# Kernel optimization log

Measured on AMD Instinct MI355X. Metric: run time of the kernel, lower is better.

## Reference

```python
import jax, jax.numpy as jnp
import numpy as np

B, S, D, H, HD, FF, L = 16384, 5, 6, 2, 3, 2048, 4
EPS = 1e-5


def setup_inputs() -> dict:
    key = jax.random.key(0)
    ks = jax.random.split(key, 20)
    s = lambda fan: 1.0 / np.sqrt(fan)
    inp = {
        'x': jax.random.normal(ks[0], (B, S, D), dtype=jnp.float32),
        # per-layer stacked MHA params (in_proj split into q/k/v) and out_proj
        'Wq': jax.random.uniform(ks[1], (L, D, D), jnp.float32, -s(D), s(D)),
        'bq': jax.random.uniform(ks[2], (L, D), jnp.float32, -s(D), s(D)),
        'Wk': jax.random.uniform(ks[3], (L, D, D), jnp.float32, -s(D), s(D)),
        'bk': jax.random.uniform(ks[4], (L, D), jnp.float32, -s(D), s(D)),
        'Wv': jax.random.uniform(ks[5], (L, D, D), jnp.float32, -s(D), s(D)),
        'bv': jax.random.uniform(ks[6], (L, D), jnp.float32, -s(D), s(D)),
        'Wo': jax.random.uniform(ks[7], (L, D, D), jnp.float32, -s(D), s(D)),
        'bo': jax.random.uniform(ks[8], (L, D), jnp.float32, -s(D), s(D)),
        # FFN: linear1 D->FF, linear2 FF->D (torch Linear stores [out,in])
        'W1': jax.random.uniform(ks[9], (L, FF, D), jnp.float32, -s(D), s(D)),
        'b1': jax.random.uniform(ks[10], (L, FF), jnp.float32, -s(D), s(D)),
        'W2': jax.random.uniform(ks[11], (L, D, FF), jnp.float32, -s(FF), s(FF)),
        'b2': jax.random.uniform(ks[12], (L, D), jnp.float32, -s(FF), s(FF)),
        # layernorms
        'g1': jnp.ones((L, D), jnp.float32),
        'be1': jnp.zeros((L, D), jnp.float32),
        'g2': jnp.ones((L, D), jnp.float32),
        'be2': jnp.zeros((L, D), jnp.float32),
        # classification head Linear(30, 2)
        'Wfc': jax.random.uniform(ks[13], (2, S * D), jnp.float32, -s(S * D), s(S * D)),
        'bfc': jax.random.uniform(ks[14], (2,), jnp.float32, -s(S * D), s(S * D)),
    }
    return inp


def _layernorm(x, g, b):
    m = jnp.mean(x, axis=-1, keepdims=True)
    v = jnp.mean(jnp.square(x - m), axis=-1, keepdims=True)
    return (x - m) * jax.lax.rsqrt(v + EPS) * g + b


def _encoder_stack(x, Wq, bq, Wk, bk, Wv, bv, Wo, bo, W1, b1, W2, b2, g1, be1, g2, be2):
    scale = 1.0 / np.sqrt(HD)
    for i in range(L):  # small fixed loop over layers
        # multi-head self-attention (post-norm, eval mode: dropout = identity)
        q = (x @ Wq[i].T + bq[i]).reshape(B, S, H, HD)
        k = (x @ Wk[i].T + bk[i]).reshape(B, S, H, HD)
        v = (x @ Wv[i].T + bv[i]).reshape(B, S, H, HD)
        scores = jnp.einsum('bqhd,bkhd->bhqk', q, k) * scale
        attn = jax.nn.softmax(scores, axis=-1)
        ctx = jnp.einsum('bhqk,bkhd->bqhd', attn, v).reshape(B, S, D)
        x = _layernorm(x + ctx @ Wo[i].T + bo[i], g1[i], be1[i])
        # FFN: relu(x W1^T + b1) W2^T + b2
        h = jax.nn.relu(x @ W1[i].T + b1[i])  # [B,S,FF]
        x = _layernorm(x + h @ W2[i].T + b2[i], g2[i], be2[i])
    return x


def reference(x, Wq, bq, Wk, bk, Wv, bv, Wo, bo, W1, b1, W2, b2, g1, be1, g2, be2, Wfc, bfc):
    t = _encoder_stack(x, Wq, bq, Wk, bk, Wv, bv, Wo, bo, W1, b1, W2, b2, g1, be1, g2, be2)
    flat = t.reshape(-1, S * D)
    logits = flat @ Wfc.T + bfc
    return jax.nn.softmax(logits, axis=1)
```

## Files before the change

### kernel.cpp

```cpp
#include <hip/hip_runtime.h>
#include <math.h>

#define NL 4
#define NBATCH 16384
#define NS 5
#define ND 6
#define NH 2
#define NHD 3
#define NFF 2048
#define EPSV 1e-5f

#define ITEMS 32
#define TPB 512
#define NPAIR 64
#define ROW (NS * ND)
#define NVAL (ITEMS * ROW)
#define HROWS 80

typedef __fp16 v8h __attribute__((ext_vector_type(8)));
typedef __fp16 v2h __attribute__((ext_vector_type(2)));
typedef float f32x4 __attribute__((ext_vector_type(4)));

union HU8 { uint4 u; v8h h; __fp16 f[8]; };

__device__ inline unsigned pk_u32(float a, float b) {
    union { v2h h; unsigned u; } x;
    x.h = __builtin_amdgcn_cvt_pkrtz(a, b);
    return x.u;
}

__device__ __align__(16) uint4 W1A[NL * NPAIR * 64];
__device__ __align__(16) uint4 W1B[NL * NPAIR * 64];
__device__ __align__(16) uint4 W2P[NL * NPAIR * 64];

__global__ void pack_kernel(const float* __restrict__ W1,
                            const float* __restrict__ b1,
                            const float* __restrict__ W2) {
    const int TOT = NL * NPAIR * 64;
    int idx = blockIdx.x * 256 + threadIdx.x;
    if (idx >= 3 * TOT) return;
    int arr = idx / TOT, t = idx - arr * TOT;
    int lane = t & 63, p = (t >> 6) & 63, l = t >> 12;
    int r = lane & 15, g = lane >> 4;
    HU8 o; o.u = make_uint4(0u, 0u, 0u, 0u);
    if (arr < 2) {
        if (g == 0) {
            int j = (2 * p + arr) * 16 + r;
#pragma unroll
            for (int e = 0; e < ND; ++e)
                o.f[e] = (__fp16)W1[(size_t)(l * NFF + j) * ND + e];
            o.f[6] = (__fp16)b1[l * NFF + j];
            o.f[7] = (__fp16)0.f;
        }
        if (arr == 0) W1A[t] = o.u; else W1B[t] = o.u;
    } else {
        if (r < ND) {
#pragma unroll
            for (int e = 0; e < 8; ++e) {
                int j = p * 32 + ((e < 4) ? (4 * g + e) : (16 + 4 * g + e - 4));
                o.f[e] = (__fp16)W2[(size_t)(l * ND + r) * NFF + j];
            }
        }
        W2P[t] = o.u;
    }
}

__global__ __launch_bounds__(TPB, 4) void encoder_kernel(
    const float* __restrict__ xin,
    const float* __restrict__ Wq, const float* __restrict__ bq,
    const float* __restrict__ Wk, const float* __restrict__ bk,
    const float* __restrict__ Wv, const float* __restrict__ bv,
    const float* __restrict__ Wo, const float* __restrict__ bo,
    const float* __restrict__ b2,
    const float* __restrict__ g1, const float* __restrict__ be1,
    const float* __restrict__ g2, const float* __restrict__ be2,
    const float* __restrict__ Wfc, const float* __restrict__ bfc,
    float* __restrict__ out) {
    __shared__ float xs[NVAL];
    __shared__ float ybuf[2 * 4 * 5 * 32 * 4];
    __shared__ float kvs[2 * 16 * NS * 12];

    const int tid = threadIdx.x;
    const int base = blockIdx.x * ITEMS;

    if (tid < NVAL / 4)
        ((float4*)xs)[tid] = ((const float4*)(xin + (size_t)base * ROW))[tid];

    const int lane = tid & 63;
    const int w = tid >> 6;
    const int jq = w & 3;
    const int c16 = lane & 15, g = lane >> 4;
    const int tid2 = tid & 255;
    const int aiL = tid2 >> 4;
    const int u = tid2 & 15;

    v8h z8; z8 = (v8h)(__fp16)0.f;
    const f32x4 cz = {0.f, 0.f, 0.f, 0.f};

    for (int k = 0; k <= 9; ++k) {
        __syncthreads();
        if (w < 4) {
            if (k >= 1 && k <= 8) {
                const int hf = (k - 1) & 1, lf = (k - 1) >> 1;
                const uint4* pw1a = W1A + (size_t)(lf * NPAIR + jq * 16) * 64 + lane;
                const uint4* pw1b = W1B + (size_t)(lf * NPAIR + jq * 16) * 64 + lane;
                const uint4* pw2  = W2P + (size_t)(lf * NPAIR + jq * 16) * 64 + lane;
                uint4 wpf[2][6];
#pragma unroll
                for (int pp = 0; pp < 2; ++pp) {
                    wpf[0][pp * 3 + 0] = pw1a[pp * 64];
                    wpf[0][pp * 3 + 1] = pw1b[pp * 64];
                    wpf[0][pp * 3 + 2] = pw2[pp * 64];
                }
                v8h xb[5];
#pragma unroll
                for (int mt = 0; mt < 5; ++mt) {
                    HU8 ux; ux.u = make_uint4(0u, 0u, 0u, 0u);
                    if (g == 0) {
                        int row = hf * HROWS + mt * 16 + c16;
                        const float* xp = &xs[row * ND];
                        ux.u.x = pk_u32(xp[0], xp[1]);
                        ux.u.y = pk_u32(xp[2], xp[3]);
                        ux.u.z = pk_u32(xp[4], xp[5]);
                        ux.u.w = 0x00003c00u;
                    }
                    xb[mt] = ux.h;
                }
                f32x4 y0 = cz, y1 = cz, y2 = cz, y3 = cz, y4 = cz;
                __builtin_amdgcn_s_setprio(1);
#pragma unroll
                for (int gq = 0; gq < 8; ++gq) {
                    const int cur = gq & 1, nxt = cur ^ 1;
                    if (gq < 7) {
#pragma unroll
                        for (int pp = 0; pp < 2; ++pp) {
                            int pofs = (gq * 2 + 2 + pp) * 64;
                            wpf[nxt][pp * 3 + 0] = pw1a[pofs];
                            wpf[nxt][pp * 3 + 1] = pw1b[pofs];
                            wpf[nxt][pp * 3 + 2] = pw2[pofs];
                        }
                    }
#pragma unroll
                    for (int pp = 0; pp < 2; ++pp) {
                        HU8 a1; a1.u = wpf[cur][pp * 3 + 0];
                        HU8 b1f; b1f.u = wpf[cur][pp * 3 + 1];
                        HU8 w2f; w2f.u = wpf[cur][pp * 3 + 2];
#define FFN_STEP(YREG, XB)                                                      \
                        {                                                       \
                            f32x4 h0 = __builtin_amdgcn_mfma_f32_16x16x32_f16(  \
                                a1.h, (XB), cz, 0, 0, 0);                       \
                            f32x4 h1 = __builtin_amdgcn_mfma_f32_16x16x32_f16(  \
                                b1f.h, (XB), cz, 0, 0, 0);                      \
                            HU8 hb;                                             \
                            hb.u.x = pk_u32(h0.x, h0.y);                        \
                            hb.u.y = pk_u32(h0.z, h0.w);                        \
                            hb.u.z = pk_u32(h1.x, h1.y);                        \
                            hb.u.w = pk_u32(h1.z, h1.w);                        \
                            hb.h = __builtin_elementwise_max(hb.h, z8);         \
                            YREG = __builtin_amdgcn_mfma_f32_16x16x32_f16(      \
                                w2f.h, hb.h, YREG, 0, 0, 0);                    \
                        }
                        FFN_STEP(y0, xb[0])
                        FFN_STEP(y1, xb[1])
                        FFN_STEP(y2, xb[2])
                        FFN_STEP(y3, xb[3])
                        FFN_STEP(y4, xb[4])
#undef FFN_STEP
                    }
                }
                __builtin_amdgcn_s_setprio(0);
                if (lane < 32) {
                    f32x4* yb4 = (f32x4*)ybuf;
                    int sb = ((hf * 4 + jq) * 5) * 32 + lane;
                    yb4[sb + 0 * 32] = y0;
                    yb4[sb + 1 * 32] = y1;
                    yb4[sb + 2 * 32] = y2;
                    yb4[sb + 3 * 32] = y3;
                    yb4[sb + 4 * 32] = y4;
                }
            }
        } else {
            if (k <= 7) {
                const int ha = k & 1, la = k >> 1;
                if (u < NS) {
                    const int ai = ha * 16 + aiL;
                    const int R = ai * NS + u;
                    const int hr = aiL * 5 + u;
                    const int mtR = hr >> 4, cR = hr & 15;
                    float xr[ND];
                    if (la == 0) {
#pragma unroll
                        for (int e = 0; e < ND; ++e) xr[e] = xs[R * ND + e];
                    } else {
                        const int lp = la - 1;
                        float yr[ND];
#pragma unroll
                        for (int d = 0; d < ND; ++d) {
                            float s = 0.f;
#pragma unroll
                            for (int q = 0; q < 4; ++q)
                                s += ybuf[(((ha * 4 + q) * 5 + mtR) * 32 +
                                           (d >> 2) * 16 + cR) * 4 + (d & 3)];
                            yr[d] = xs[R * ND + d] + s + b2[lp * ND + d];
                        }
                        float m = 0.f;
#pragma unroll
                        for (int d = 0; d < ND; ++d) m += yr[d];
                        m *= (1.f / ND);
                        float va = 0.f;
#pragma unroll
                        for (int d = 0; d < ND; ++d) { float dv = yr[d] - m; va += dv * dv; }
                        va *= (1.f / ND);
                        float r = rsqrtf(va + EPSV);
#pragma unroll
                        for (int d = 0; d < ND; ++d)
                            xr[d] = (yr[d] - m) * r * g2[lp * ND + d] + be2[lp * ND + d];
                    }
                    float qr[ND], kr[ND], vr[ND];
#pragma unroll
                    for (int d = 0; d < ND; ++d) {
                        float aq = bq[la * ND + d], ak = bk[la * ND + d], av = bv[la * ND + d];
#pragma unroll
                        for (int e = 0; e < ND; ++e) {
                            aq += Wq[(la * ND + d) * ND + e] * xr[e];
                            ak += Wk[(la * ND + d) * ND + e] * xr[e];
                            av += Wv[(la * ND + d) * ND + e] * xr[e];
                        }
                        qr[d] = aq; kr[d] = ak; vr[d] = av;
                    }
                    const int gb = (ha * 16 + aiL) * NS;
#pragma unroll
                    for (int d = 0; d < ND; ++d) {
                        kvs[(gb + u) * 12 + d] = kr[d];
                        kvs[(gb + u) * 12 + 6 + d] = vr[d];
                    }
                    __builtin_amdgcn_wave_barrier();
                    const float scale = 0.57735026919f;
                    float cf[ND];
#pragma unroll
                    for (int h = 0; h < NH; ++h) {
                        float sc[NS];
                        float mx = -1e30f;
#pragma unroll
                        for (int u2 = 0; u2 < NS; ++u2) {
                            float s = 0.f;
#pragma unroll
                            for (int c = 0; c < NHD; ++c)
                                s += qr[h * NHD + c] * kvs[(gb + u2) * 12 + h * NHD + c];
                            s *= scale;
                            sc[u2] = s;
                            mx = fmaxf(mx, s);
                        }
                        float sum = 0.f;
#pragma unroll
                        for (int u2 = 0; u2 < NS; ++u2) { sc[u2] = __expf(sc[u2] - mx); sum += sc[u2]; }
                        float inv = 1.f / sum;
#pragma unroll
                        for (int c = 0; c < NHD; ++c) {
                            float cx = 0.f;
#pragma unroll
                            for (int u2 = 0; u2 < NS; ++u2)
                                cx += sc[u2] * kvs[(gb + u2) * 12 + 6 + h * NHD + c];
                            cf[h * NHD + c] = cx * inv;
                        }
                    }
                    float yo[ND];
#pragma unroll
                    for (int d = 0; d < ND; ++d) {
                        float a = bo[la * ND + d];
#pragma unroll
                        for (int e = 0; e < ND; ++e) a += Wo[(la * ND + d) * ND + e] * cf[e];
                        yo[d] = a + xr[d];
                    }
                    float m1 = 0.f;
#pragma unroll
                    for (int d = 0; d < ND; ++d) m1 += yo[d];
                    m1 *= (1.f / ND);
                    float v1 = 0.f;
#pragma unroll
                    for (int d = 0; d < ND; ++d) { float dv = yo[d] - m1; v1 += dv * dv; }
                    v1 *= (1.f / ND);
                    float r1 = rsqrtf(v1 + EPSV);
#pragma unroll
                    for (int d = 0; d < ND; ++d)
                        xs[R * ND + d] = (yo[d] - m1) * r1 * g1[la * ND + d] + be1[la * ND + d];
                }
            } else {
                const int hd = k & 1;
                if (u < 2) {
                    const int ai = hd * 16 + aiL;
                    float acc = bfc[u];
#pragma unroll
                    for (int t = 0; t < NS; ++t) {
                        const int R = ai * NS + t;
                        const int hr = aiL * 5 + t;
                        const int mtR = hr >> 4, cR = hr & 15;
                        float yr[ND];
#pragma unroll
                        for (int d = 0; d < ND; ++d) {
                            float s = 0.f;
#pragma unroll
                            for (int q = 0; q < 4; ++q)
                                s += ybuf[(((hd * 4 + q) * 5 + mtR) * 32 +
                                           (d >> 2) * 16 + cR) * 4 + (d & 3)];
                            yr[d] = xs[R * ND + d] + s + b2[3 * ND + d];
                        }
                        float m = 0.f;
#pragma unroll
                        for (int d = 0; d < ND; ++d) m += yr[d];
                        m *= (1.f / ND);
                        float va = 0.f;
#pragma unroll
                        for (int d = 0; d < ND; ++d) { float dv = yr[d] - m; va += dv * dv; }
                        va *= (1.f / ND);
                        float r = rsqrtf(va + EPSV);
#pragma unroll
                        for (int d = 0; d < ND; ++d) {
                            float xv = (yr[d] - m) * r * g2[3 * ND + d] + be2[3 * ND + d];
                            acc += Wfc[u * ROW + t * ND + d] * xv;
                        }
                    }
                    kvs[(hd * 16 + aiL) * 12 + u] = acc;
                    __builtin_amdgcn_wave_barrier();
                    float l0 = kvs[(hd * 16 + aiL) * 12 + 0];
                    float l1 = kvs[(hd * 16 + aiL) * 12 + 1];
                    float mxv = fmaxf(l0, l1);
                    float e0 = __expf(l0 - mxv), e1 = __expf(l1 - mxv);
                    float pv = (u == 0) ? (e0 / (e0 + e1)) : (e1 / (e0 + e1));
                    out[(size_t)(base + ai) * 2 + u] = pv;
                }
            }
        }
    }
}

extern "C" void kernel_launch(void* const* d_in, const int* in_sizes, int n_in,
                              void* d_out, int out_size, void* d_ws, size_t ws_size,
                              hipStream_t stream) {
    (void)in_sizes; (void)n_in; (void)d_ws; (void)ws_size; (void)out_size;
    const float* x = (const float*)d_in[0];
    const float* Wq = (const float*)d_in[1];
    const float* bq = (const float*)d_in[2];
    const float* Wk = (const float*)d_in[3];
    const float* bk = (const float*)d_in[4];
    const float* Wv = (const float*)d_in[5];
    const float* bv = (const float*)d_in[6];
    const float* Wo = (const float*)d_in[7];
    const float* bo = (const float*)d_in[8];
    const float* W1 = (const float*)d_in[9];
    const float* b1 = (const float*)d_in[10];
    const float* W2 = (const float*)d_in[11];
    const float* b2 = (const float*)d_in[12];
    const float* g1 = (const float*)d_in[13];
    const float* be1 = (const float*)d_in[14];
    const float* g2 = (const float*)d_in[15];
    const float* be2 = (const float*)d_in[16];
    const float* Wfc = (const float*)d_in[17];
    const float* bfc = (const float*)d_in[18];
    float* out = (float*)d_out;

    const int npack = 3 * NL * NPAIR * 64;
    hipLaunchKernelGGL(pack_kernel, dim3((npack + 255) / 256), dim3(256), 0, stream,
                       W1, b1, W2);
    hipLaunchKernelGGL(encoder_kernel, dim3(NBATCH / ITEMS), dim3(TPB), 0, stream,
                       x, Wq, bq, Wk, bk, Wv, bv, Wo, bo, b2, g1, be1, g2, be2,
                       Wfc, bfc, out);
}
```

Measured before the change: 76.27 us.

## Replace warp-specialized attention/FFN pipeline with all-warp per-layer phases

The old kernel split the block into four FFN waves and four attention waves and ran a 10-step software pipeline over two half-batches, so attention of one half overlapped the FFN of the other. The new kernel drops that specialization. All eight waves do attention for all 32 items, split per head across 10 lanes per item, then all eight waves run the FFN MFMAs, each wave covering one of two 80-row groups. This doubles the waves issuing MFMAs and spreads the attention work more evenly, but it gives up the overlap between attention and FFN and adds more block-wide barriers per layer.

```diff
diff --git a/kernel.cpp b/kernel.cpp
--- a/kernel.cpp
+++ b/kernel.cpp
@@ -15,7 +15,6 @@
 #define NPAIR 64
 #define ROW (NS * ND)
 #define NVAL (ITEMS * ROW)
-#define HROWS 80
 
 typedef __fp16 v8h __attribute__((ext_vector_type(8)));
 typedef __fp16 v2h __attribute__((ext_vector_type(2)));
@@ -77,260 +76,235 @@
     const float* __restrict__ Wfc, const float* __restrict__ bfc,
     float* __restrict__ out) {
     __shared__ float xs[NVAL];
-    __shared__ float ybuf[2 * 4 * 5 * 32 * 4];
-    __shared__ float kvs[2 * 16 * NS * 12];
+    __shared__ float ybuf[4 * 2 * 5 * 32 * 4];
+    __shared__ float kvs[ITEMS * NS * 12];
+    __shared__ float cxs[ITEMS * 10 * 3];
 
     const int tid = threadIdx.x;
     const int base = blockIdx.x * ITEMS;
 
     if (tid < NVAL / 4)
         ((float4*)xs)[tid] = ((const float4*)(xin + (size_t)base * ROW))[tid];
+    __syncthreads();
 
     const int lane = tid & 63;
     const int w = tid >> 6;
-    const int jq = w & 3;
+    const int jq = w & 3, ig = w >> 2;
     const int c16 = lane & 15, g = lane >> 4;
-    const int tid2 = tid & 255;
-    const int aiL = tid2 >> 4;
-    const int u = tid2 & 15;
+    const int ai = tid >> 4;
+    const int u = tid & 15;
+    const int at = u >> 1, hh = u & 1;
 
     v8h z8; z8 = (v8h)(__fp16)0.f;
     const f32x4 cz = {0.f, 0.f, 0.f, 0.f};
 
-    for (int k = 0; k <= 9; ++k) {
+    for (int l = 0; l < NL; ++l) {
+        const uint4* pw1a = W1A + (size_t)(l * NPAIR + jq * 16) * 64 + lane;
+        const uint4* pw1b = W1B + (size_t)(l * NPAIR + jq * 16) * 64 + lane;
+        const uint4* pw2  = W2P + (size_t)(l * NPAIR + jq * 16) * 64 + lane;
+        uint4 wpf[2][6];
+#pragma unroll
+        for (int pp = 0; pp < 2; ++pp) {
+            wpf[0][pp * 3 + 0] = pw1a[pp * 64];
+            wpf[0][pp * 3 + 1] = pw1b[pp * 64];
+            wpf[0][pp * 3 + 2] = pw2[pp * 64];
+        }
+        float xr[ND], qh[NHD];
+        if (u < 10) {
+            const int R = ai * NS + at;
+#pragma unroll
+            for (int e = 0; e < ND; ++e) xr[e] = xs[R * ND + e];
+            float kh[NHD], vh[NHD];
+#pragma unroll
+            for (int c = 0; c < NHD; ++c) {
+                int d = hh * NHD + c;
+                float aq = bq[l * ND + d], ak = bk[l * ND + d], av = bv[l * ND + d];
+#pragma unroll
+                for (int e = 0; e < ND; ++e) {
+                    aq += Wq[(l * ND + d) * ND + e] * xr[e];
+                    ak += Wk[(l * ND + d) * ND + e] * xr[e];
+                    av += Wv[(l * ND + d) * ND + e] * xr[e];
+                }
+                qh[c] = aq; kh[c] = ak; vh[c] = av;
+            }
+#pragma unroll
+            for (int c = 0; c < NHD; ++c) {
+                kvs[(ai * NS + at) * 12 + hh * NHD + c] = kh[c];
+                kvs[(ai * NS + at) * 12 + 6 + hh * NHD + c] = vh[c];
+            }
+        }
+        __builtin_amdgcn_wave_barrier();
+        if (u < 10) {
+            const float scale = 0.57735026919f;
+            float sc[NS], mx = -1e30f;
+#pragma unroll
+            for (int u2 = 0; u2 < NS; ++u2) {
+                float s = 0.f;
+#pragma unroll
+                for (int c = 0; c < NHD; ++c)
+                    s += qh[c] * kvs[(ai * NS + u2) * 12 + hh * NHD + c];
+                s *= scale;
+                sc[u2] = s;
+                mx = fmaxf(mx, s);
+            }
+            float sum = 0.f;
+#pragma unroll
+            for (int u2 = 0; u2 < NS; ++u2) { sc[u2] = __expf(sc[u2] - mx); sum += sc[u2]; }
+            float inv = 1.f / sum;
+#pragma unroll
+            for (int c = 0; c < NHD; ++c) {
+                float cx = 0.f;
+#pragma unroll
+                for (int u2 = 0; u2 < NS; ++u2)
+                    cx += sc[u2] * kvs[(ai * NS + u2) * 12 + 6 + hh * NHD + c];
+                cxs[(ai * 10 + u) * 3 + c] = cx * inv;
+            }
+        }
+        __builtin_amdgcn_wave_barrier();
+        if (u < 10) {
+            const int R = ai * NS + at;
+            float cf[ND];
+#pragma unroll
+            for (int c = 0; c < NHD; ++c) {
+                cf[hh * NHD + c] = cxs[(ai * 10 + u) * 3 + c];
+                cf[(1 - hh) * NHD + c] = cxs[(ai * 10 + at * 2 + (1 - hh)) * 3 + c];
+            }
+            float yo[ND];
+#pragma unroll
+            for (int d = 0; d < ND; ++d) {
+                float a = bo[l * ND + d];
+#pragma unroll
+                for (int e = 0; e < ND; ++e) a += Wo[(l * ND + d) * ND + e] * cf[e];
+                yo[d] = a + xr[d];
+            }
+            float m1 = 0.f;
+#pragma unroll
+            for (int d = 0; d < ND; ++d) m1 += yo[d];
+            m1 *= (1.f / ND);
+            float v1 = 0.f;
+#pragma unroll
+            for (int d = 0; d < ND; ++d) { float dv = yo[d] - m1; v1 += dv * dv; }
+            v1 *= (1.f / ND);
+            float r1 = rsqrtf(v1 + EPSV);
+#pragma unroll
+            for (int c = 0; c < NHD; ++c) {
+                int d = hh * NHD + c;
+                xs[R * ND + d] = (yo[d] - m1) * r1 * g1[l * ND + d] + be1[l * ND + d];
+            }
+        }
         __syncthreads();
-        if (w < 4) {
-            if (k >= 1 && k <= 8) {
-                const int hf = (k - 1) & 1, lf = (k - 1) >> 1;
-                const uint4* pw1a = W1A + (size_t)(lf * NPAIR + jq * 16) * 64 + lane;
-                const uint4* pw1b = W1B + (size_t)(lf * NPAIR + jq * 16) * 64 + lane;
-                const uint4* pw2  = W2P + (size_t)(lf * NPAIR + jq * 16) * 64 + lane;
-                uint4 wpf[2][6];
+        v8h xb[5];
+#pragma unroll
+        for (int mt = 0; mt < 5; ++mt) {
+            HU8 ux; ux.u = make_uint4(0u, 0u, 0u, 0u);
+            if (g == 0) {
+                int row = ig * 80 + mt * 16 + c16;
+                const float* xp = &xs[row * ND];
+                ux.u.x = pk_u32(xp[0], xp[1]);
+                ux.u.y = pk_u32(xp[2], xp[3]);
+                ux.u.z = pk_u32(xp[4], xp[5]);
+                ux.u.w = 0x00003c00u;
+            }
+            xb[mt] = ux.h;
+        }
+        f32x4 y0 = cz, y1 = cz, y2 = cz, y3 = cz, y4 = cz;
+        __builtin_amdgcn_s_setprio(1);
+#pragma unroll
+        for (int gq = 0; gq < 8; ++gq) {
+            const int cur = gq & 1, nxt = cur ^ 1;
+            if (gq < 7) {
 #pragma unroll
                 for (int pp = 0; pp < 2; ++pp) {
-                    wpf[0][pp * 3 + 0] = pw1a[pp * 64];
-                    wpf[0][pp * 3 + 1] = pw1b[pp * 64];
-                    wpf[0][pp * 3 + 2] = pw2[pp * 64];
+                    int pofs = (gq * 2 + 2 + pp) * 64;
+                    wpf[nxt][pp * 3 + 0] = pw1a[pofs];
+                    wpf[nxt][pp * 3 + 1] = pw1b[pofs];
+                    wpf[nxt][pp * 3 + 2] = pw2[pofs];
                 }
-                v8h xb[5];
-#pragma unroll
-                for (int mt = 0; mt < 5; ++mt) {
-                    HU8 ux; ux.u = make_uint4(0u, 0u, 0u, 0u);
-                    if (g == 0) {
-                        int row = hf * HROWS + mt * 16 + c16;
-                        const float* xp = &xs[row * ND];
-                        ux.u.x = pk_u32(xp[0], xp[1]);
-                        ux.u.y = pk_u32(xp[2], xp[3]);
-                        ux.u.z = pk_u32(xp[4], xp[5]);
-                        ux.u.w = 0x00003c00u;
-                    }
-                    xb[mt] = ux.h;
+            }
+#pragma unroll
+            for (int pp = 0; pp < 2; ++pp) {
+                HU8 a1; a1.u = wpf[cur][pp * 3 + 0];
+                HU8 b1f; b1f.u = wpf[cur][pp * 3 + 1];
+                HU8 w2f; w2f.u = wpf[cur][pp * 3 + 2];
+#define FFN_STEP(YREG, XB)                                                      \
+                {                                                               \
+                    f32x4 h0 = __builtin_amdgcn_mfma_f32_16x16x32_f16(          \
+                        a1.h, (XB), cz, 0, 0, 0);                               \
+                    f32x4 h1 = __builtin_amdgcn_mfma_f32_16x16x32_f16(          \
+                        b1f.h, (XB), cz, 0, 0, 0);                              \
+                    HU8 hb;                                                     \
+                    hb.u.x = pk_u32(h0.x, h0.y);                                \
+                    hb.u.y = pk_u32(h0.z, h0.w);                                \
+                    hb.u.z = pk_u32(h1.x, h1.y);                                \
+                    hb.u.w = pk_u32(h1.z, h1.w);                                \
+                    hb.h = __builtin_elementwise_max(hb.h, z8);                 \
+                    YREG = __builtin_amdgcn_mfma_f32_16x16x32_f16(              \
+                        w2f.h, hb.h, YREG, 0, 0, 0);                            \
                 }
-                f32x4 y0 = cz, y1 = cz, y2 = cz, y3 = cz, y4 = cz;
-                __builtin_amdgcn_s_setprio(1);
-#pragma unroll
-                for (int gq = 0; gq < 8; ++gq) {
-                    const int cur = gq & 1, nxt = cur ^ 1;
-                    if (gq < 7) {
-#pragma unroll
-                        for (int pp = 0; pp < 2; ++pp) {
-                            int pofs = (gq * 2 + 2 + pp) * 64;
-                            wpf[nxt][pp * 3 + 0] = pw1a[pofs];
-                            wpf[nxt][pp * 3 + 1] = pw1b[pofs];
-                            wpf[nxt][pp * 3 + 2] = pw2[pofs];
-                        }
-                    }
-#pragma unroll
-                    for (int pp = 0; pp < 2; ++pp) {
-                        HU8 a1; a1.u = wpf[cur][pp * 3 + 0];
-                        HU8 b1f; b1f.u = wpf[cur][pp * 3 + 1];
-                        HU8 w2f; w2f.u = wpf[cur][pp * 3 + 2];
-#define FFN_STEP(YREG, XB)                                                      \
-                        {                                                       \
-                            f32x4 h0 = __builtin_amdgcn_mfma_f32_16x16x32_f16(  \
-                                a1.h, (XB), cz, 0, 0, 0);                       \
-                            f32x4 h1 = __builtin_amdgcn_mfma_f32_16x16x32_f16(  \
-                                b1f.h, (XB), cz, 0, 0, 0);                      \
-                            HU8 hb;                                             \
-                            hb.u.x = pk_u32(h0.x, h0.y);                        \
-                            hb.u.y = pk_u32(h0.z, h0.w);                        \
-                            hb.u.z = pk_u32(h1.x, h1.y);                        \
-                            hb.u.w = pk_u32(h1.z, h1.w);                        \
-                            hb.h = __builtin_elementwise_max(hb.h, z8);         \
-                            YREG = __builtin_amdgcn_mfma_f32_16x16x32_f16(      \
-                                w2f.h, hb.h, YREG, 0, 0, 0);                    \
-                        }
-                        FFN_STEP(y0, xb[0])
-                        FFN_STEP(y1, xb[1])
-                        FFN_STEP(y2, xb[2])
-                        FFN_STEP(y3, xb[3])
-                        FFN_STEP(y4, xb[4])
+                FFN_STEP(y0, xb[0])
+                FFN_STEP(y1, xb[1])
+                FFN_STEP(y2, xb[2])
+                FFN_STEP(y3, xb[3])
+                FFN_STEP(y4, xb[4])
 #undef FFN_STEP
-                    }
-                }
-                __builtin_amdgcn_s_setprio(0);
-                if (lane < 32) {
-                    f32x4* yb4 = (f32x4*)ybuf;
-                    int sb = ((hf * 4 + jq) * 5) * 32 + lane;
-                    yb4[sb + 0 * 32] = y0;
-                    yb4[sb + 1 * 32] = y1;
-                    yb4[sb + 2 * 32] = y2;
-                    yb4[sb + 3 * 32] = y3;
-                    yb4[sb + 4 * 32] = y4;
-                }
-            }
-        } else {
-            if (k <= 7) {
-                const int ha = k & 1, la = k >> 1;
-                if (u < NS) {
-                    const int ai = ha * 16 + aiL;
-                    const int R = ai * NS + u;
-                    const int hr = aiL * 5 + u;
-                    const int mtR = hr >> 4, cR = hr & 15;
-                    float xr[ND];
-                    if (la == 0) {
-#pragma unroll
-                        for (int e = 0; e < ND; ++e) xr[e] = xs[R * ND + e];
-                    } else {
-                        const int lp = la - 1;
-                        float yr[ND];
-#pragma unroll
-                        for (int d = 0; d < ND; ++d) {
-                            float s = 0.f;
-#pragma unroll
-                            for (int q = 0; q < 4; ++q)
-                                s += ybuf[(((ha * 4 + q) * 5 + mtR) * 32 +
-                                           (d >> 2) * 16 + cR) * 4 + (d & 3)];
-                            yr[d] = xs[R * ND + d] + s + b2[lp * ND + d];
-                        }
-                        float m = 0.f;
-#pragma unroll
-                        for (int d = 0; d < ND; ++d) m += yr[d];
-                        m *= (1.f / ND);
-                        float va = 0.f;
-#pragma unroll
-                        for (int d = 0; d < ND; ++d) { float dv = yr[d] - m; va += dv * dv; }
-                        va *= (1.f / ND);
-                        float r = rsqrtf(va + EPSV);
-#pragma unroll
-                        for (int d = 0; d < ND; ++d)
-                            xr[d] = (yr[d] - m) * r * g2[lp * ND + d] + be2[lp * ND + d];
-                    }
-                    float qr[ND], kr[ND], vr[ND];
-#pragma unroll
-                    for (int d = 0; d < ND; ++d) {
-                        float aq = bq[la * ND + d], ak = bk[la * ND + d], av = bv[la * ND + d];
-#pragma unroll
-                        for (int e = 0; e < ND; ++e) {
-                            aq += Wq[(la * ND + d) * ND + e] * xr[e];
-                            ak += Wk[(la * ND + d) * ND + e] * xr[e];
-                            av += Wv[(la * ND + d) * ND + e] * xr[e];
-                        }
-                        qr[d] = aq; kr[d] = ak; vr[d] = av;
-                    }
-                    const int gb = (ha * 16 + aiL) * NS;
-#pragma unroll
-                    for (int d = 0; d < ND; ++d) {
-                        kvs[(gb + u) * 12 + d] = kr[d];
-                        kvs[(gb + u) * 12 + 6 + d] = vr[d];
-                    }
-                    __builtin_amdgcn_wave_barrier();
-                    const float scale = 0.57735026919f;
-                    float cf[ND];
-#pragma unroll
-                    for (int h = 0; h < NH; ++h) {
-                        float sc[NS];
-                        float mx = -1e30f;
-#pragma unroll
-                        for (int u2 = 0; u2 < NS; ++u2) {
-                            float s = 0.f;
-#pragma unroll
-                            for (int c = 0; c < NHD; ++c)
-                                s += qr[h * NHD + c] * kvs[(gb + u2) * 12 + h * NHD + c];
-                            s *= scale;
-                            sc[u2] = s;
-                            mx = fmaxf(mx, s);
-                        }
-                        float sum = 0.f;
-#pragma unroll
-                        for (int u2 = 0; u2 < NS; ++u2) { sc[u2] = __expf(sc[u2] - mx); sum += sc[u2]; }
-                        float inv = 1.f / sum;
-#pragma unroll
-                        for (int c = 0; c < NHD; ++c) {
-                            float cx = 0.f;
-#pragma unroll
-                            for (int u2 = 0; u2 < NS; ++u2)
-                                cx += sc[u2] * kvs[(gb + u2) * 12 + 6 + h * NHD + c];
-                            cf[h * NHD + c] = cx * inv;
-                        }
-                    }
-                    float yo[ND];
-#pragma unroll
-                    for (int d = 0; d < ND; ++d) {
-                        float a = bo[la * ND + d];
-#pragma unroll
-                        for (int e = 0; e < ND; ++e) a += Wo[(la * ND + d) * ND + e] * cf[e];
-                        yo[d] = a + xr[d];
-                    }
-                    float m1 = 0.f;
-#pragma unroll
-                    for (int d = 0; d < ND; ++d) m1 += yo[d];
-                    m1 *= (1.f / ND);
-                    float v1 = 0.f;
-#pragma unroll
-                    for (int d = 0; d < ND; ++d) { float dv = yo[d] - m1; v1 += dv * dv; }
-                    v1 *= (1.f / ND);
-                    float r1 = rsqrtf(v1 + EPSV);
-#pragma unroll
-                    for (int d = 0; d < ND; ++d)
-                        xs[R * ND + d] = (yo[d] - m1) * r1 * g1[la * ND + d] + be1[la * ND + d];
-                }
-            } else {
-                const int hd = k & 1;
-                if (u < 2) {
-                    const int ai = hd * 16 + aiL;
-                    float acc = bfc[u];
-#pragma unroll
-                    for (int t = 0; t < NS; ++t) {
-                        const int R = ai * NS + t;
-                        const int hr = aiL * 5 + t;
-                        const int mtR = hr >> 4, cR = hr & 15;
-                        float yr[ND];
-#pragma unroll
-                        for (int d = 0; d < ND; ++d) {
-                            float s = 0.f;
-#pragma unroll
-                            for (int q = 0; q < 4; ++q)
-                                s += ybuf[(((hd * 4 + q) * 5 + mtR) * 32 +
-                                           (d >> 2) * 16 + cR) * 4 + (d & 3)];
-                            yr[d] = xs[R * ND + d] + s + b2[3 * ND + d];
-                        }
-                        float m = 0.f;
-#pragma unroll
-                        for (int d = 0; d < ND; ++d) m += yr[d];
-                        m *= (1.f / ND);
-                        float va = 0.f;
-#pragma unroll
-                        for (int d = 0; d < ND; ++d) { float dv = yr[d] - m; va += dv * dv; }
-                        va *= (1.f / ND);
-                        float r = rsqrtf(va + EPSV);
-#pragma unroll
-                        for (int d = 0; d < ND; ++d) {
-                            float xv = (yr[d] - m) * r * g2[3 * ND + d] + be2[3 * ND + d];
-                            acc += Wfc[u * ROW + t * ND + d] * xv;
-                        }
-                    }
-                    kvs[(hd * 16 + aiL) * 12 + u] = acc;
-                    __builtin_amdgcn_wave_barrier();
-                    float l0 = kvs[(hd * 16 + aiL) * 12 + 0];
-                    float l1 = kvs[(hd * 16 + aiL) * 12 + 1];
-                    float mxv = fmaxf(l0, l1);
-                    float e0 = __expf(l0 - mxv), e1 = __expf(l1 - mxv);
-                    float pv = (u == 0) ? (e0 / (e0 + e1)) : (e1 / (e0 + e1));
-                    out[(size_t)(base + ai) * 2 + u] = pv;
-                }
-            }
-        }
+            }
+        }
+        __builtin_amdgcn_s_setprio(0);
+        if (lane < 32) {
+            f32x4* yb4 = (f32x4*)ybuf;
+            int sb = ((jq * 2 + ig) * 5) * 32 + lane;
+            yb4[sb + 0 * 32] = y0;
+            yb4[sb + 1 * 32] = y1;
+            yb4[sb + 2 * 32] = y2;
+            yb4[sb + 3 * 32] = y3;
+            yb4[sb + 4 * 32] = y4;
+        }
+        __syncthreads();
+        if (u < NS) {
+            const int R = ai * NS + u;
+            const int hr = (ai & 15) * 5 + u;
+            const int mtR = hr >> 4, cR = hr & 15;
+            const int igA = ai >> 4;
+            float yr[ND];
+#pragma unroll
+            for (int d = 0; d < ND; ++d) {
+                float s = 0.f;
+#pragma unroll
+                for (int q = 0; q < 4; ++q)
+                    s += ybuf[(((q * 2 + igA) * 5 + mtR) * 32 +
+                               (d >> 2) * 16 + cR) * 4 + (d & 3)];
+                yr[d] = xs[R * ND + d] + s + b2[l * ND + d];
+            }
+            float m = 0.f;
+#pragma unroll
+            for (int d = 0; d < ND; ++d) m += yr[d];
+            m *= (1.f / ND);
+            float va = 0.f;
+#pragma unroll
+            for (int d = 0; d < ND; ++d) { float dv = yr[d] - m; va += dv * dv; }
+            va *= (1.f / ND);
+            float r = rsqrtf(va + EPSV);
+#pragma unroll
+            for (int d = 0; d < ND; ++d)
+                xs[R * ND + d] = (yr[d] - m) * r * g2[l * ND + d] + be2[l * ND + d];
+        }
+        __builtin_amdgcn_wave_barrier();
+    }
+    if (u < 2) {
+        float acc = bfc[u];
+#pragma unroll
+        for (int v = 0; v < ROW; ++v)
+            acc += Wfc[u * ROW + v] * xs[ai * ROW + v];
+        cxs[(ai * 10 + u) * 3] = acc;
+    }
+    __builtin_amdgcn_wave_barrier();
+    if (u < 2) {
+        float l0 = cxs[(ai * 10 + 0) * 3];
+        float l1 = cxs[(ai * 10 + 1) * 3];
+        float mxv = fmaxf(l0, l1);
+        float e0 = __expf(l0 - mxv), e1 = __expf(l1 - mxv);
+        float pv = (u == 0) ? (e0 / (e0 + e1)) : (e1 / (e0 + e1));
+        out[(size_t)(base + ai) * 2 + u] = pv;
     }
 }
 
```

New measurement: 75.53 us. No clear change (-1.0%).
